# Optimization experiments

Hardware: AMD Instinct MI355X
Metric: run time of the kernel (lower is better)

Reference implementation:

```python
import jax, jax.numpy as jnp
import numpy as np

B, N, S = 32, 1000, 200
D, H, DK, FF, NL = 128, 8, 16, 512, 3
HK = H * DK


def _mha(x, Wq, Wk, Wv, Wo, bo):
    # x: [B, L, D]; manual multi-head attention matching the torch code
    Bv, L, _ = x.shape
    q = (x @ Wq).reshape(Bv, L, H, DK).transpose(0, 2, 1, 3)  # [B,H,L,dk]
    k = (x @ Wk).reshape(Bv, L, H, DK).transpose(0, 2, 1, 3)
    v = (x @ Wv).reshape(Bv, L, H, DK).transpose(0, 2, 1, 3)
    score = jnp.einsum('bhid,bhjd->bhij', q, k) / jnp.sqrt(jnp.asarray(DK, x.dtype))
    w = jax.nn.softmax(score, axis=-1)
    o = jnp.einsum('bhij,bhjd->bhid', w, v).transpose(0, 2, 1, 3).reshape(Bv, L, HK)
    return o @ Wo + bo


def _decoder_layer(x, Wq, Wk, Wv, Wo, bo, W1, b1, W2, b2):
    out1 = x + _mha(x, Wq, Wk, Wv, Wo, bo)
    ff = jax.nn.relu(out1 @ W1 + b1) @ W2 + b2
    return out1 + ff


def _forward(data, attention_bias, Wfirst, bfirst, Wlast, blast,
             Wq, Wk, Wv, Wo, bo, W1, b1, W2, b2, Wfin, bfin, sel):
    Bv, Np, Dm = data.shape
    Sn = sel.shape[1]
    bidx = jnp.arange(Bv)
    # _get_new_data: ordered list of unselected node indices, shape [B, N-S]
    mask = jnp.zeros((Bv, Np), bool).at[bidx[:, None], sel].set(True)
    vals = jnp.where(mask, Np, jnp.arange(Np)[None, :])
    unselect = jnp.sort(vals, axis=1)[:, : Np - Sn]            # [B, N-S]
    left = jnp.take_along_axis(data, unselect[:, :, None], axis=1)  # [B, N-S, D]
    # _get_encoding for first / last selected node
    first = data[bidx, sel[:, 0]]
    last = data[bidx, sel[:, -1]]
    ef = first @ Wfirst + bfirst
    el = last @ Wlast + blast
    out = jnp.concatenate([ef[:, None], left, el[:, None]], axis=1)  # [B, N-S+2, D]
    for i in range(Wq.shape[0]):
        out = _decoder_layer(out, Wq[i], Wk[i], Wv[i], Wo[i], bo[i],
                             W1[i], b1[i], W2[i], b2[i])
    logits = (out @ Wfin + bfin)[..., 0]                       # [B, N-S+2]
    # attention bias of current (last selected) node, gathered at unselected
    ab_cur = attention_bias[bidx, sel[:, -1]]                  # [B, N]
    ab_uns = jnp.take_along_axis(ab_cur, unselect, axis=1)     # [B, N-S]
    logits = logits.at[:, 1:-1].add(ab_uns)
    L = logits.shape[1]
    pos = jnp.arange(L)
    end_mask = (pos == 0) | (pos == L - 1)
    logits = jnp.where(end_mask[None, :], -jnp.inf, logits)
    props = jax.nn.softmax(logits, axis=-1)[:, 1:-1]           # [B, N-S]
    props = jnp.where(props <= 1e-5, props + 1e-7, props)
    # scatter back: selected positions -> -2, unselected -> props
    new_props = jnp.full((Bv, Np), -2.0, dtype=data.dtype)
    new_props = new_props.at[bidx[:, None], unselect].set(props)
    return new_props


def setup_inputs() -> dict:
    key = jax.random.key(0)
    ks = jax.random.split(key, 24)
    data = jax.random.normal(ks[0], (B, N, D), jnp.float32)
    # selected_node_list must contain unique indices per row (partial tour)
    sel = jax.vmap(lambda k: jax.random.permutation(k, N))(
        jax.random.split(ks[1], B))[:, :S].astype(jnp.int32)
    attention_bias = jax.random.normal(ks[2], (B, N, N), jnp.float32)

    def lin(k, shape, fan_in):
        return jax.random.normal(k, shape, jnp.float32) / np.float32(np.sqrt(fan_in))

    return dict(
        data=data,
        attention_bias=attention_bias,
        Wfirst=lin(ks[3], (D, D), D), bfirst=jnp.zeros((D,), jnp.float32),
        Wlast=lin(ks[4], (D, D), D), blast=jnp.zeros((D,), jnp.float32),
        Wq=lin(ks[5], (NL, D, HK), D),
        Wk=lin(ks[6], (NL, D, HK), D),
        Wv=lin(ks[7], (NL, D, HK), D),
        Wo=lin(ks[8], (NL, HK, D), HK), bo=jnp.zeros((NL, D), jnp.float32),
        W1=lin(ks[9], (NL, D, FF), D), b1=jnp.zeros((NL, FF), jnp.float32),
        W2=lin(ks[10], (NL, FF, D), FF), b2=jnp.zeros((NL, D), jnp.float32),
        Wfin=lin(ks[11], (D, 1), D), bfin=jnp.zeros((1,), jnp.float32),
        selected_node_list=sel,
    )


def reference(data, attention_bias, Wfirst, bfirst, Wlast, blast,
              Wq, Wk, Wv, Wo, bo, W1, b1, W2, b2, Wfin, bfin,
              selected_node_list):
    return _forward(data, attention_bias, Wfirst, bfirst, Wlast, blast,
                    Wq, Wk, Wv, Wo, bo, W1, b1, W2, b2, Wfin, bfin,
                    selected_node_list)
```

## Files before the change

kernel.cpp:

```cpp
#include <hip/hip_runtime.h>
#include <hip/hip_bf16.h>
#include <math.h>

#define NB 32
#define NN 1000
#define SS 200
#define DD 128
#define HH 8
#define DKK 16
#define FFD 512
#define NLAYER 3
#define LQ 802
#define LPAD 832
#define NPADK (LPAD - LQ)
#define MROWS (NB*LQ)
#define NBLK64 (MROWS/64)
#define NQT 26
#define NQT64 13
#define HSTR 516
#define TSTR 132
#define QSCALE 0.3606737602f

typedef __attribute__((ext_vector_type(8))) short short8;
typedef __attribute__((ext_vector_type(4))) short short4v;
typedef __attribute__((ext_vector_type(16))) float f32x16;
typedef __attribute__((ext_vector_type(2))) unsigned int uint2v;

static __device__ __forceinline__ unsigned short f2bf(float x) {
  union { float f; unsigned int u; } v; v.f = x;
  unsigned int r = v.u + 0x7fff + ((v.u >> 16) & 1);
  return (unsigned short)(r >> 16);
}

static __device__ __forceinline__ unsigned short f2bf1(float x) {
  unsigned int r;
  asm("v_cvt_pk_bf16_f32 %0, %1, 0" : "=v"(r) : "v"(x));
  return (unsigned short)r;
}

static __device__ __forceinline__ unsigned int cvtpk_bf16(float lo, float hi) {
  unsigned int r;
  asm("v_cvt_pk_bf16_f32 %0, %1, %2" : "=v"(r) : "v"(lo), "v"(hi));
  return r;
}

static __device__ __forceinline__ float max3f(float a, float b, float c) {
  float r;
  asm("v_max3_f32 %0, %1, %2, %3" : "=v"(r) : "v"(a), "v"(b), "v"(c));
  return r;
}

static __device__ __forceinline__ float exp2n(float x) {
  float r;
  asm("v_exp_f32 %0, %1" : "=v"(r) : "v"(x));
  return r;
}

static __device__ __forceinline__ uint2v pls(unsigned int a, unsigned int b) {
  return __builtin_amdgcn_permlane32_swap(a, b, false, false);
}
static __device__ __forceinline__ unsigned int fu(float x){ return __float_as_uint(x); }
static __device__ __forceinline__ float uf(unsigned int x){ return __uint_as_float(x); }

#define WCH 196608
__global__ __launch_bounds__(256) void k_wconv(const float* __restrict__ Wq, const float* __restrict__ Wk,
                       const float* __restrict__ Wv, const float* __restrict__ Wo,
                       const float* __restrict__ W1, const float* __restrict__ W2,
                       unsigned short* __restrict__ WtQKV, unsigned short* __restrict__ Wot,
                       unsigned short* __restrict__ W1t, unsigned short* __restrict__ W2t) {
  int e = blockIdx.x*256 + threadIdx.x;
  if (e >= 3*WCH) return;
  int layer = e / WCH, r = e - layer*WCH;
  if (r < 49152) {
    int n = r >> 7, k = r & 127;
    int sect = n >> 7, nn = n & 127;
    const float* W = (sect == 0) ? Wq : (sect == 1) ? Wk : Wv;
    WtQKV[layer*49152 + r] = f2bf1(W[layer*16384 + k*128 + nn]);
  } else if (r < 65536) {
    int r2 = r - 49152;
    int n = r2 >> 7, k = r2 & 127;
    Wot[layer*16384 + r2] = f2bf1(Wo[layer*16384 + k*128 + n]);
  } else if (r < 131072) {
    int r2 = r - 65536;
    int n = r2 >> 7, k = r2 & 127;
    W1t[layer*65536 + r2] = f2bf1(W1[layer*65536 + k*512 + n]);
  } else {
    int r2 = r - 131072;
    int n = r2 >> 9, k = r2 & 511;
    W2t[layer*65536 + r2] = f2bf1(W2[layer*65536 + k*128 + n]);
  }
}

__global__ __launch_bounds__(256) void k_padzero(unsigned short* __restrict__ Kb,
                                                 unsigned short* __restrict__ Vt) {
  int e = blockIdx.x*256 + threadIdx.x;
  if (e < 61440) {
    int bh = e / 240, r = e - bh*240;
    ((unsigned int*)&Kb[((size_t)bh*LPAD + LQ)*DKK])[r] = 0u;
  } else {
    int e2 = e - 61440;
    int bh = e2 / 240, r = e2 - bh*240;
    int d = r / 15, li = r - d*15;
    ((unsigned int*)&Vt[((size_t)bh*DKK + d)*LPAD + LQ])[li] = 0u;
  }
}

__global__ __launch_bounds__(1024) void k_unselect(const int* __restrict__ sel,
                                                   int* __restrict__ unselect,
                                                   int* __restrict__ pos) {
  int b = blockIdx.x;
  int n = threadIdx.x;
  __shared__ unsigned char fl[1024];
  __shared__ int wsum[16];
  fl[n] = (n < NN) ? 1 : 0;
  __syncthreads();
  if (n < SS) fl[sel[b*SS + n]] = 0;
  __syncthreads();
  int flag = fl[n];
  unsigned long long m = __ballot(flag);
  int lane = n & 63, w = n >> 6;
  int pre = __popcll(m & ((1ULL << lane) - 1ULL));
  if (lane == 63) wsum[w] = pre + flag;
  __syncthreads();
  int off = 0;
  #pragma unroll
  for (int i = 0; i < 16; ++i) off += (i < w) ? wsum[i] : 0;
  if (n < NN) {
    if (flag) {
      int j = off + pre;
      unselect[b*800 + j] = n;
      pos[b*NN + n] = j + 1;
    } else {
      pos[b*NN + n] = -1;
    }
  }
}

__global__ __launch_bounds__(128) void k_embed_ends(const float* __restrict__ data,
                       const int* __restrict__ sel,
                       const float* __restrict__ Wfirst, const float* __restrict__ bfirst,
                       const float* __restrict__ Wlast, const float* __restrict__ blast,
                       float* __restrict__ X, unsigned short* __restrict__ Xbf) {
  int which = blockIdx.x, b = blockIdx.y, d = threadIdx.x;
  int l = (which == 0) ? 0 : LQ-1;
  __shared__ float xr[DD];
  int src = sel[b*SS + (which == 0 ? 0 : SS-1)];
  const float* W    = (which == 0) ? Wfirst : Wlast;
  const float* bias = (which == 0) ? bfirst : blast;
  xr[d] = data[((size_t)b*NN + src)*DD + d];
  __syncthreads();
  float acc = bias[d];
  #pragma unroll 4
  for (int k = 0; k < DD; ++k) acc += xr[k] * W[k*DD + d];
  size_t off = ((size_t)(b*LQ + l))*DD + d;
  X[off] = acc;
  Xbf[off] = f2bf1(acc);
}

__global__ __launch_bounds__(256) void k_embed_mid(const float* __restrict__ data,
                       const int* __restrict__ unselect,
                       float* __restrict__ X, unsigned short* __restrict__ Xbf) {
  int e = blockIdx.x*256 + threadIdx.x;
  int r = e >> 5;
  int c4 = (e & 31) * 4;
  int b = r / 800, j = r - b*800;
  int nidx = unselect[r];
  const float4 v = *(const float4*)&data[((size_t)b*NN + nidx)*DD + c4];
  size_t off = ((size_t)(b*LQ + 1 + j))*DD + c4;
  *(float4*)&X[off] = v;
  unsigned int lo = cvtpk_bf16(v.x, v.y);
  unsigned int hi = cvtpk_bf16(v.z, v.w);
  unsigned long long pk8 = ((unsigned long long)hi << 32) | (unsigned long long)lo;
  *(unsigned long long*)&Xbf[off] = pk8;
}

__global__ __launch_bounds__(256) void k_qkv_mfma(const unsigned short* __restrict__ Xbf,
                       const unsigned short* __restrict__ Wt,
                       unsigned short* __restrict__ Qb, unsigned short* __restrict__ Kb,
                       unsigned short* __restrict__ Vt) {
  int row0 = blockIdx.x * 64;
  int t = threadIdx.x, wave = t >> 6, lane = t & 63;
  int col = lane & 31, half = lane >> 5;
  int b0 = row0 / LQ;
  int l00 = row0 - b0*LQ;
  int split = LQ - l00;
  short8 a[2][8];
  const unsigned short* xb = Xbf + (size_t)(row0 + col)*DD + half*8;
  #pragma unroll
  for (int mi = 0; mi < 2; ++mi)
    #pragma unroll
    for (int s = 0; s < 8; ++s)
      a[mi][s] = *(const short8*)(xb + (size_t)mi*32*DD + s*16);
  #pragma unroll
  for (int nn = 0; nn < 3; ++nn) {
    int ni = wave*3 + nn;
    short8 bfr[8];
    const unsigned short* wb = Wt + (size_t)(ni*32 + col)*DD + half*8;
    #pragma unroll
    for (int s = 0; s < 8; ++s) bfr[s] = *(const short8*)(wb + s*16);
    f32x16 acc0 = {0.f,0.f,0.f,0.f,0.f,0.f,0.f,0.f,0.f,0.f,0.f,0.f,0.f,0.f,0.f,0.f};
    f32x16 acc1 = {0.f,0.f,0.f,0.f,0.f,0.f,0.f,0.f,0.f,0.f,0.f,0.f,0.f,0.f,0.f,0.f};
    #pragma unroll
    for (int s = 0; s < 8; ++s) {
      acc0 = __builtin_amdgcn_mfma_f32_32x32x16_bf16(a[0][s], bfr[s], acc0, 0, 0, 0);
      acc1 = __builtin_amdgcn_mfma_f32_32x32x16_bf16(a[1][s], bfr[s], acc1, 0, 0, 0);
    }
    int n = ni*32 + col;
    int sect = n >> 7, nc = n & 127;
    int h = nc >> 4, d = nc & 15;
    if (sect < 2) {
      #pragma unroll
      for (int mi = 0; mi < 2; ++mi) {
        const f32x16& acc = mi ? acc1 : acc0;
        #pragma unroll
        for (int r = 0; r < 16; ++r) {
          int ml = mi*32 + (r&3) + 8*(r>>2) + 4*half;
          int over = (ml >= split);
          int b_ = b0 + over;
          int l  = over ? (ml - split) : (l00 + ml);
          size_t bh = (size_t)(b_*HH + h);
          float v = acc[r];
          if (sect == 0) Qb[(bh*LPAD + l)*DKK + d] = f2bf1(v * QSCALE);
          else           Kb[(bh*LPAD + l)*DKK + d] = f2bf1(v);
        }
      }
    } else {
      #pragma unroll
      for (int mi = 0; mi < 2; ++mi) {
        const f32x16& acc = mi ? acc1 : acc0;
        #pragma unroll
        for (int pj = 0; pj < 8; ++pj) {
          int j = pj >> 1, pi = pj & 1;
          int mlp = mi*32 + 8*j + 4*half + 2*pi;
          int over = (mlp >= split);
          int b_ = b0 + over;
          int l  = over ? (mlp - split) : (l00 + mlp);
          unsigned int w = cvtpk_bf16(acc[4*j + 2*pi], acc[4*j + 2*pi + 1]);
          *(unsigned int*)&Vt[((size_t)(b_*HH + h)*DKK + d)*LPAD + l] = w;
        }
      }
    }
  }
}

__global__ __launch_bounds__(256) void k_attn3(const unsigned short* __restrict__ Q,
                       const unsigned short* __restrict__ K,
                       const unsigned short* __restrict__ Vt,
                       unsigned short* __restrict__ Obf) {
  int bid = blockIdx.x;
  int g = bid & 7, i = bid >> 3;
  int bhg = i / NQT64, qt = i - bhg*NQT64;
  int bh = bhg*8 + g;
  int b = bh >> 3, h = bh & 7;
  int q0 = qt*64;
  size_t bhL = (size_t)bh * LPAD;
  int t = threadIdx.x;
  int wave = t >> 6, lane = t & 63;
  int col = lane & 31;
  int half = lane >> 5;

  __shared__ float mw[2][4][32];
  __shared__ float sw[2][4][32];
  __shared__ float sfin[2][32];
  __shared__ float ored[2][4][16][32];
  __shared__ float osum[2][32][17];

  uint2v pr = pls(1000u + (unsigned)lane, 2000u + (unsigned)lane);
  bool case1 = (__builtin_amdgcn_readfirstlane((int)pr.x) >= 2000);

  int q0c = q0 + col;      if (q0c > LQ-1) q0c = LQ-1;
  int q1c = q0 + 32 + col; if (q1c > LQ-1) q1c = LQ-1;
  short8 bQ0 = *(const short8*)&Q[(bhL + q0c)*DKK + half*8];
  short8 bQ1 = *(const short8*)&Q[(bhL + q1c)*DKK + half*8];

  f32x16 oacc0 = {0.f,0.f,0.f,0.f,0.f,0.f,0.f,0.f,0.f,0.f,0.f,0.f,0.f,0.f,0.f,0.f};
  f32x16 oacc1 = oacc0;
  float runm0 = 0.f, runm1 = 0.f;
  bool act = false;

  short8 aV0 = {0,0,0,0,0,0,0,0};
  short8 aV1 = {0,0,0,0,0,0,0,0};
  if (col == 16) {
    union { unsigned int u[4]; short8 s8; } o;
    o.u[0] = o.u[1] = o.u[2] = o.u[3] = 0x3F803F80u;
    aV0 = o.s8; aV1 = o.s8;
  }

  for (int kt = wave; kt < NQT; kt += 4) {
    int key0 = kt*32;
    short8 aK = *(const short8*)&K[(bhL + key0 + col)*DKK + half*8];
    if (col < 16) {
      const unsigned short* vp = &Vt[((size_t)bh*DKK + col)*LPAD + key0 + half*8];
      aV0 = *(const short8*)vp;
      aV1 = *(const short8*)(vp + 16);
    }

    auto process = [&](const short8& bQ, f32x16& oacc, float& runm) {
      f32x16 c = {0.f,0.f,0.f,0.f,0.f,0.f,0.f,0.f,0.f,0.f,0.f,0.f,0.f,0.f,0.f,0.f};
      c = __builtin_amdgcn_mfma_f32_32x32x16_bf16(aK, bQ, c, 0, 0, 0);
      float m0 = max3f(c[0],  c[1],  c[2]);
      float m1 = max3f(c[3],  c[4],  c[5]);
      float m2 = max3f(c[6],  c[7],  c[8]);
      float m3 = max3f(c[9],  c[10], c[11]);
      float m4 = max3f(c[12], c[13], c[14]);
      float tm = fmaxf(max3f(m0, m1, m2), max3f(m3, m4, c[15]));
      if (!__all(tm <= runm + 80.0f)) {
        uint2v rr = pls(fu(tm), fu(tm));
        float tmp = max3f(tm, uf(rr.x), uf(rr.y));
        float mnew = fmaxf(runm, tmp);
        float sc = exp2n(runm - mnew);
        #pragma unroll
        for (int r = 0; r < 9; ++r) oacc[r] *= sc;
        runm = mnew;
        act = true;
      }
      float p[16];
      if (act) {
        #pragma unroll
        for (int r = 0; r < 16; ++r) p[r] = exp2n(c[r] - runm);
      } else {
        #pragma unroll
        for (int r = 0; r < 16; ++r) p[r] = exp2n(c[r]);
      }
      unsigned int pk[8];
      #pragma unroll
      for (int j = 0; j < 8; ++j) pk[j] = cvtpk_bf16(p[2*j], p[2*j+1]);
      unsigned int fAx, fAy, fAz, fAw, fBx, fBy, fBz, fBw;
      if (case1) {
        uint2v r0 = pls(pk[2], pk[0]); fAz = r0.x; fAx = r0.y;
        uint2v r1 = pls(pk[3], pk[1]); fAw = r1.x; fAy = r1.y;
        uint2v r2 = pls(pk[6], pk[4]); fBz = r2.x; fBx = r2.y;
        uint2v r3 = pls(pk[7], pk[5]); fBw = r3.x; fBy = r3.y;
      } else {
        uint2v r0 = pls(pk[0], pk[2]); fAx = r0.x; fAz = r0.y;
        uint2v r1 = pls(pk[1], pk[3]); fAy = r1.x; fAw = r1.y;
        uint2v r2 = pls(pk[4], pk[6]); fBx = r2.x; fBz = r2.y;
        uint2v r3 = pls(pk[5], pk[7]); fBy = r3.x; fBw = r3.y;
      }
      union { unsigned int u[4]; short8 s8; } fA, fB;
      fA.u[0] = fAx; fA.u[1] = fAy; fA.u[2] = fAz; fA.u[3] = fAw;
      fB.u[0] = fBx; fB.u[1] = fBy; fB.u[2] = fBz; fB.u[3] = fBw;
      oacc = __builtin_amdgcn_mfma_f32_32x32x16_bf16(aV0, fA.s8, oacc, 0, 0, 0);
      oacc = __builtin_amdgcn_mfma_f32_32x32x16_bf16(aV1, fB.s8, oacc, 0, 0, 0);
    };
    process(bQ0, oacc0, runm0);
    process(bQ1, oacc1, runm1);
  }

  if (half == 0) {
    mw[0][wave][col] = runm0;  sw[0][wave][col] = oacc0[8];
    mw[1][wave][col] = runm1;  sw[1][wave][col] = oacc1[8];
  }
  __syncthreads();
  #pragma unroll
  for (int u = 0; u < 2; ++u) {
    float M = fmaxf(fmaxf(mw[u][0][col], mw[u][1][col]), fmaxf(mw[u][2][col], mw[u][3][col]));
    float S = sw[u][0][col]*exp2n(mw[u][0][col]-M) + sw[u][1][col]*exp2n(mw[u][1][col]-M)
            + sw[u][2][col]*exp2n(mw[u][2][col]-M) + sw[u][3][col]*exp2n(mw[u][3][col]-M);
    float runm = u ? runm1 : runm0;
    float fw = exp2n(runm - M);
    const f32x16& oacc = u ? oacc1 : oacc0;
    #pragma unroll
    for (int r = 0; r < 8; ++r) {
      int dv = (r&3) + 8*(r>>2) + 4*half;
      ored[u][wave][dv][col] = oacc[r] * fw;
    }
    if (wave == 0 && half == 0)
      sfin[u][col] = S - (float)NPADK * exp2n(-M);
  }
  __syncthreads();
  {
    int qq = t & 31, dv0 = t >> 5;
    #pragma unroll
    for (int u = 0; u < 2; ++u)
      #pragma unroll
      for (int k = 0; k < 2; ++k) {
        int dv = dv0 + 8*k;
        osum[u][qq][dv] = ored[u][0][dv][qq] + ored[u][1][dv][qq]
                        + ored[u][2][dv][qq] + ored[u][3][dv][qq];
      }
  }
  __syncthreads();
  {
    int qs = t >> 3, c2 = (t & 7)*2;
    #pragma unroll
    for (int u = 0; u < 2; ++u) {
      int q = q0 + u*32 + qs;
      if (q < LQ) {
        float invS = 1.f / sfin[u][qs];
        unsigned int pkv = cvtpk_bf16(osum[u][qs][c2] * invS, osum[u][qs][c2+1] * invS);
        *(unsigned int*)&Obf[((size_t)(b*LQ + q))*DD + h*DKK + c2] = pkv;
      }
    }
  }
}

__global__ __launch_bounds__(256) void k_pff(const unsigned short* __restrict__ Obf,
        const unsigned short* __restrict__ Wot, const float* __restrict__ bo,
        const unsigned short* __restrict__ W1t, const float* __restrict__ b1,
        const unsigned short* __restrict__ W2t, const float* __restrict__ b2,
        float* __restrict__ X, unsigned short* __restrict__ Xbf) {
  __shared__ __align__(16) unsigned short LDSU[64 * HSTR];
  unsigned short* T  = LDSU;
  unsigned short* Hs = LDSU;
  int row0 = blockIdx.x * 64;
  int t = threadIdx.x, wave = t >> 6, lane = t & 63;
  int col = lane & 31, half = lane >> 5;
  int n = wave*32 + col;
  float res[2][16];
  {
    short8 a[2][8];
    const unsigned short* ob = Obf + (size_t)(row0 + col)*DD + half*8;
    #pragma unroll
    for (int mi = 0; mi < 2; ++mi)
      #pragma unroll
      for (int s = 0; s < 8; ++s)
        a[mi][s] = *(const short8*)(ob + (size_t)mi*32*DD + s*16);
    short8 bfr[8];
    const unsigned short* wb = Wot + (size_t)n*DD + half*8;
    #pragma unroll
    for (int s = 0; s < 8; ++s) bfr[s] = *(const short8*)(wb + s*16);
    f32x16 acc0 = {0.f,0.f,0.f,0.f,0.f,0.f,0.f,0.f,0.f,0.f,0.f,0.f,0.f,0.f,0.f,0.f};
    f32x16 acc1 = acc0;
    #pragma unroll
    for (int s = 0; s < 8; ++s) {
      acc0 = __builtin_amdgcn_mfma_f32_32x32x16_bf16(a[0][s], bfr[s], acc0, 0, 0, 0);
      acc1 = __builtin_amdgcn_mfma_f32_32x32x16_bf16(a[1][s], bfr[s], acc1, 0, 0, 0);
    }
    float bv = bo[n];
    #pragma unroll
    for (int mi = 0; mi < 2; ++mi) {
      const f32x16& acc = mi ? acc1 : acc0;
      #pragma unroll
      for (int r = 0; r < 16; ++r) {
        int ml = mi*32 + (r&3) + 8*(r>>2) + 4*half;
        size_t off = (size_t)(row0 + ml)*DD + n;
        res[mi][r] = X[off] + acc[r] + bv;
        T[ml*TSTR + n] = f2bf1(res[mi][r]);
      }
    }
  }
  __syncthreads();
  short8 aF[2][8];
  #pragma unroll
  for (int mi = 0; mi < 2; ++mi)
    #pragma unroll
    for (int s = 0; s < 8; ++s) {
      const unsigned short* tp = &T[(mi*32 + col)*TSTR + half*8 + s*16];
      union { short4v h[2]; short8 v; } u;
      u.h[0] = *(const short4v*)tp;
      u.h[1] = *(const short4v*)(tp + 4);
      aF[mi][s] = u.v;
    }
  __syncthreads();
  #pragma unroll
  for (int nn = 0; nn < 4; ++nn) {
    int ni = wave*4 + nn;
    short8 bfr[8];
    const unsigned short* wb = W1t + (size_t)(ni*32 + col)*DD + half*8;
    #pragma unroll
    for (int s = 0; s < 8; ++s) bfr[s] = *(const short8*)(wb + s*16);
    f32x16 acc0 = {0.f,0.f,0.f,0.f,0.f,0.f,0.f,0.f,0.f,0.f,0.f,0.f,0.f,0.f,0.f,0.f};
    f32x16 acc1 = acc0;
    #pragma unroll
    for (int s = 0; s < 8; ++s) {
      acc0 = __builtin_amdgcn_mfma_f32_32x32x16_bf16(aF[0][s], bfr[s], acc0, 0, 0, 0);
      acc1 = __builtin_amdgcn_mfma_f32_32x32x16_bf16(aF[1][s], bfr[s], acc1, 0, 0, 0);
    }
    int nf = ni*32 + col;
    float bv = b1[nf];
    #pragma unroll
    for (int mi = 0; mi < 2; ++mi) {
      const f32x16& acc = mi ? acc1 : acc0;
      #pragma unroll
      for (int r = 0; r < 16; ++r) {
        int ml = mi*32 + (r&3) + 8*(r>>2) + 4*half;
        Hs[ml*HSTR + nf] = f2bf1(fmaxf(acc[r] + bv, 0.f));
      }
    }
  }
  __syncthreads();
  f32x16 acc0 = {0.f,0.f,0.f,0.f,0.f,0.f,0.f,0.f,0.f,0.f,0.f,0.f,0.f,0.f,0.f,0.f};
  f32x16 acc1 = acc0;
  const unsigned short* w2b = W2t + (size_t)n*FFD + half*8;
  #pragma unroll 4
  for (int s = 0; s < 32; ++s) {
    int ko = s*16 + half*8;
    union { short4v h[2]; short8 v; } h0, h1;
    const unsigned short* hp0 = &Hs[col*HSTR + ko];
    const unsigned short* hp1 = &Hs[(32 + col)*HSTR + ko];
    h0.h[0] = *(const short4v*)hp0;  h0.h[1] = *(const short4v*)(hp0 + 4);
    h1.h[0] = *(const short4v*)hp1;  h1.h[1] = *(const short4v*)(hp1 + 4);
    short8 bfr = *(const short8*)(w2b + s*16);
    acc0 = __builtin_amdgcn_mfma_f32_32x32x16_bf16(h0.v, bfr, acc0, 0, 0, 0);
    acc1 = __builtin_amdgcn_mfma_f32_32x32x16_bf16(h1.v, bfr, acc1, 0, 0, 0);
  }
  float bv = b2[n];
  #pragma unroll
  for (int mi = 0; mi < 2; ++mi) {
    const f32x16& acc = mi ? acc1 : acc0;
    #pragma unroll
    for (int r = 0; r < 16; ++r) {
      int ml = mi*32 + (r&3) + 8*(r>>2) + 4*half;
      size_t off = (size_t)(row0 + ml)*DD + n;
      float v = res[mi][r] + acc[r] + bv;
      X[off] = v;
      Xbf[off] = f2bf1(v);
    }
  }
}

__global__ __launch_bounds__(256) void k_final(const float* __restrict__ X,
                       const float* __restrict__ Wfin, const float* __restrict__ bfin,
                       const float* __restrict__ AB, const int* __restrict__ sel,
                       const int* __restrict__ unselect, const int* __restrict__ pos,
                       float* __restrict__ out) {
  int b = blockIdx.x, t = threadIdx.x;
  __shared__ float sl[800];
  __shared__ float red[256];
  __shared__ float wf[DD];
  if (t < DD) wf[t] = Wfin[t];
  int lastsel = sel[b*SS + SS-1];
  const float* abrow = AB + ((size_t)b*NN + lastsel)*NN;
  float bias = bfin[0];
  __syncthreads();
  for (int j = t; j < 800; j += 256) {
    const float* xr = &X[((size_t)(b*LQ + 1 + j))*DD];
    float acc = 0.f;
    #pragma unroll 8
    for (int k = 0; k < DD; k += 4) {
      float4 xv = *(const float4*)&xr[k];
      acc += xv.x*wf[k] + xv.y*wf[k+1] + xv.z*wf[k+2] + xv.w*wf[k+3];
    }
    sl[j] = acc + bias + abrow[unselect[b*800 + j]];
  }
  __syncthreads();
  float lm = -INFINITY;
  for (int j = t; j < 800; j += 256) lm = fmaxf(lm, sl[j]);
  red[t] = lm;
  __syncthreads();
  for (int s = 128; s > 0; s >>= 1) {
    if (t < s) red[t] = fmaxf(red[t], red[t+s]);
    __syncthreads();
  }
  float m = red[0];
  __syncthreads();
  float ls = 0.f;
  for (int j = t; j < 800; j += 256) ls += __expf(sl[j] - m);
  red[t] = ls;
  __syncthreads();
  for (int s = 128; s > 0; s >>= 1) {
    if (t < s) red[t] += red[t+s];
    __syncthreads();
  }
  float inv = 1.f / red[0];
  for (int n = t; n < NN; n += 256) {
    int p1 = pos[b*NN + n];
    float v = -2.0f;
    if (p1 >= 0) {
      float p = __expf(sl[p1-1] - m) * inv;
      if (p <= 1e-5f) p += 1e-7f;
      v = p;
    }
    out[(size_t)b*NN + n] = v;
  }
}

extern "C" void kernel_launch(void* const* d_in, const int* in_sizes, int n_in,
                              void* d_out, int out_size, void* d_ws, size_t ws_size,
                              hipStream_t stream) {
  const float* data   = (const float*)d_in[0];
  const float* AB     = (const float*)d_in[1];
  const float* Wfirst = (const float*)d_in[2];
  const float* bfirst = (const float*)d_in[3];
  const float* Wlast  = (const float*)d_in[4];
  const float* blast  = (const float*)d_in[5];
  const float* Wq     = (const float*)d_in[6];
  const float* Wk     = (const float*)d_in[7];
  const float* Wv     = (const float*)d_in[8];
  const float* Wo     = (const float*)d_in[9];
  const float* bo     = (const float*)d_in[10];
  const float* W1     = (const float*)d_in[11];
  const float* b1     = (const float*)d_in[12];
  const float* W2     = (const float*)d_in[13];
  const float* b2     = (const float*)d_in[14];
  const float* Wfin   = (const float*)d_in[15];
  const float* bfin   = (const float*)d_in[16];
  const int*   sel    = (const int*)d_in[17];
  float* out = (float*)d_out;
  (void)in_sizes; (void)n_in; (void)out_size; (void)ws_size;

  char* ws = (char*)d_ws;
  const size_t NELT = (size_t)MROWS * DD;
  const size_t KVELT = (size_t)NB*HH*LPAD*DKK;
  int*   UNSEL = (int*)ws;
  int*   POS   = (int*)(ws + 102400);
  float* X     = (float*)(ws + 230400);
  unsigned short* Xbf = (unsigned short*)(X + NELT);
  unsigned short* Ob  = Xbf + NELT;
  unsigned short* Qb  = Ob + NELT;
  unsigned short* Kb  = Qb + KVELT;
  unsigned short* Vt  = Kb + KVELT;
  unsigned short* WtQKV = Vt + KVELT;
  unsigned short* Wot = WtQKV + (size_t)NLAYER*384*128;
  unsigned short* W1t = Wot + (size_t)NLAYER*128*128;
  unsigned short* W2t = W1t + (size_t)NLAYER*512*128;

  k_wconv<<<(3*WCH + 255)/256, 256, 0, stream>>>(Wq, Wk, Wv, Wo, W1, W2, WtQKV, Wot, W1t, W2t);
  k_padzero<<<480, 256, 0, stream>>>(Kb, Vt);
  k_unselect<<<NB, 1024, 0, stream>>>(sel, UNSEL, POS);
  k_embed_ends<<<dim3(2, NB), 128, 0, stream>>>(data, sel, Wfirst, bfirst, Wlast, blast, X, Xbf);
  k_embed_mid<<<3200, 256, 0, stream>>>(data, UNSEL, X, Xbf);
  for (int i = 0; i < NLAYER; ++i) {
    k_qkv_mfma<<<NBLK64, 256, 0, stream>>>(Xbf, WtQKV + (size_t)i*384*128, Qb, Kb, Vt);
    k_attn3<<<NQT64*HH*NB, 256, 0, stream>>>(Qb, Kb, Vt, Ob);
    k_pff<<<NBLK64, 256, 0, stream>>>(Ob, Wot + (size_t)i*128*128, bo + (size_t)i*DD,
                                      W1t + (size_t)i*512*128, b1 + (size_t)i*FFD,
                                      W2t + (size_t)i*128*512, b2 + (size_t)i*DD, X, Xbf);
  }
  k_final<<<NB, 256, 0, stream>>>(X, Wfin, bfin, AB, sel, UNSEL, POS, out);
}
```

Measured before the change: 534.0 us.

## Give each attention wave its own query tile and halve PFF row block

The attention kernel now assigns each wave a separate 64-query tile that loops over all key tiles. Previously the four waves split the keys and merged partial softmax state through shared memory with three barriers; now normalization is done per wave in registers with a lane-pair permute and only a wave-local LDS transpose for coalesced stores. The feed-forward kernel processes 32 rows per block instead of 64, doubling the grid and shrinking LDS and register use. The trade-off is less K/V reuse per wave, idle trailing waves in the last query block, and reloading the weight tiles twice as often in the feed-forward kernel.

```diff
diff --git a/kernel.cpp b/kernel.cpp
--- a/kernel.cpp
+++ b/kernel.cpp
@@ -15,8 +15,8 @@
 #define NPADK (LPAD - LQ)
 #define MROWS (NB*LQ)
 #define NBLK64 (MROWS/64)
+#define NBLK32 (MROWS/32)
 #define NQT 26
-#define NQT64 13
 #define HSTR 516
 #define TSTR 132
 #define QSCALE 0.3606737602f
@@ -249,27 +249,25 @@
                        unsigned short* __restrict__ Obf) {
   int bid = blockIdx.x;
   int g = bid & 7, i = bid >> 3;
-  int bhg = i / NQT64, qt = i - bhg*NQT64;
+  int bhg = i >> 2, qb = i & 3;
   int bh = bhg*8 + g;
   int b = bh >> 3, h = bh & 7;
-  int q0 = qt*64;
   size_t bhL = (size_t)bh * LPAD;
   int t = threadIdx.x;
   int wave = t >> 6, lane = t & 63;
   int col = lane & 31;
   int half = lane >> 5;
 
-  __shared__ float mw[2][4][32];
-  __shared__ float sw[2][4][32];
-  __shared__ float sfin[2][32];
-  __shared__ float ored[2][4][16][32];
-  __shared__ float osum[2][32][17];
+  __shared__ __align__(16) unsigned short SO[4][2][32][20];
+
+  int q0w = qb*256 + wave*64;
+  if (q0w >= LPAD) return;
 
   uint2v pr = pls(1000u + (unsigned)lane, 2000u + (unsigned)lane);
   bool case1 = (__builtin_amdgcn_readfirstlane((int)pr.x) >= 2000);
 
-  int q0c = q0 + col;      if (q0c > LQ-1) q0c = LQ-1;
-  int q1c = q0 + 32 + col; if (q1c > LQ-1) q1c = LQ-1;
+  int q0c = q0w + col;      if (q0c > LQ-1) q0c = LQ-1;
+  int q1c = q0w + 32 + col; if (q1c > LQ-1) q1c = LQ-1;
   short8 bQ0 = *(const short8*)&Q[(bhL + q0c)*DKK + half*8];
   short8 bQ1 = *(const short8*)&Q[(bhL + q1c)*DKK + half*8];
 
@@ -286,7 +284,7 @@
     aV0 = o.s8; aV1 = o.s8;
   }
 
-  for (int kt = wave; kt < NQT; kt += 4) {
+  for (int kt = 0; kt < NQT; ++kt) {
     int key0 = kt*32;
     short8 aK = *(const short8*)&K[(bhL + key0 + col)*DKK + half*8];
     if (col < 16) {
@@ -347,52 +345,36 @@
     process(bQ1, oacc1, runm1);
   }
 
-  if (half == 0) {
-    mw[0][wave][col] = runm0;  sw[0][wave][col] = oacc0[8];
-    mw[1][wave][col] = runm1;  sw[1][wave][col] = oacc1[8];
-  }
-  __syncthreads();
   #pragma unroll
   for (int u = 0; u < 2; ++u) {
-    float M = fmaxf(fmaxf(mw[u][0][col], mw[u][1][col]), fmaxf(mw[u][2][col], mw[u][3][col]));
-    float S = sw[u][0][col]*exp2n(mw[u][0][col]-M) + sw[u][1][col]*exp2n(mw[u][1][col]-M)
-            + sw[u][2][col]*exp2n(mw[u][2][col]-M) + sw[u][3][col]*exp2n(mw[u][3][col]-M);
+    const f32x16& oacc = u ? oacc1 : oacc0;
     float runm = u ? runm1 : runm0;
-    float fw = exp2n(runm - M);
-    const f32x16& oacc = u ? oacc1 : oacc0;
-    #pragma unroll
-    for (int r = 0; r < 8; ++r) {
-      int dv = (r&3) + 8*(r>>2) + 4*half;
-      ored[u][wave][dv][col] = oacc[r] * fw;
-    }
-    if (wave == 0 && half == 0)
-      sfin[u][col] = S - (float)NPADK * exp2n(-M);
-  }
-  __syncthreads();
-  {
-    int qq = t & 31, dv0 = t >> 5;
-    #pragma unroll
-    for (int u = 0; u < 2; ++u)
-      #pragma unroll
-      for (int k = 0; k < 2; ++k) {
-        int dv = dv0 + 8*k;
-        osum[u][qq][dv] = ored[u][0][dv][qq] + ored[u][1][dv][qq]
-                        + ored[u][2][dv][qq] + ored[u][3][dv][qq];
-      }
-  }
-  __syncthreads();
-  {
-    int qs = t >> 3, c2 = (t & 7)*2;
-    #pragma unroll
-    for (int u = 0; u < 2; ++u) {
-      int q = q0 + u*32 + qs;
-      if (q < LQ) {
-        float invS = 1.f / sfin[u][qs];
-        unsigned int pkv = cvtpk_bf16(osum[u][qs][c2] * invS, osum[u][qs][c2+1] * invS);
-        *(unsigned int*)&Obf[((size_t)(b*LQ + q))*DD + h*DKK + c2] = pkv;
-      }
-    }
-  }
+    uint2v re = pls(fu(oacc[8]), fu(oacc[8]));
+    float S = uf(re.x) + uf(re.y) - (float)NPADK * exp2n(-runm);
+    float invS = 1.f / S;
+    unsigned int o0 = cvtpk_bf16(oacc[0]*invS, oacc[1]*invS);
+    unsigned int o1 = cvtpk_bf16(oacc[2]*invS, oacc[3]*invS);
+    unsigned int o2 = cvtpk_bf16(oacc[4]*invS, oacc[5]*invS);
+    unsigned int o3 = cvtpk_bf16(oacc[6]*invS, oacc[7]*invS);
+    int dbase = 4*half;
+    *(unsigned int*)&SO[wave][u][col][dbase+0]  = o0;
+    *(unsigned int*)&SO[wave][u][col][dbase+2]  = o1;
+    *(unsigned int*)&SO[wave][u][col][dbase+8]  = o2;
+    *(unsigned int*)&SO[wave][u][col][dbase+10] = o3;
+  }
+  asm volatile("s_waitcnt lgkmcnt(0)" ::: "memory");
+  __builtin_amdgcn_sched_barrier(0);
+  #pragma unroll
+  for (int u = 0; u < 2; ++u)
+    #pragma unroll
+    for (int pass = 0; pass < 2; ++pass) {
+      int qq = pass*16 + (lane >> 2);
+      int s = lane & 3;
+      ushort4 v = *(const ushort4*)&SO[wave][u][qq][s*4];
+      int q = q0w + u*32 + qq;
+      if (q < LQ)
+        *(ushort4*)&Obf[((size_t)(b*LQ + q))*DD + h*DKK + s*4] = v;
+    }
 }
 
 __global__ __launch_bounds__(256) void k_pff(const unsigned short* __restrict__ Obf,
@@ -400,58 +382,47 @@
         const unsigned short* __restrict__ W1t, const float* __restrict__ b1,
         const unsigned short* __restrict__ W2t, const float* __restrict__ b2,
         float* __restrict__ X, unsigned short* __restrict__ Xbf) {
-  __shared__ __align__(16) unsigned short LDSU[64 * HSTR];
+  __shared__ __align__(16) unsigned short LDSU[32 * HSTR];
   unsigned short* T  = LDSU;
   unsigned short* Hs = LDSU;
-  int row0 = blockIdx.x * 64;
+  int row0 = blockIdx.x * 32;
   int t = threadIdx.x, wave = t >> 6, lane = t & 63;
   int col = lane & 31, half = lane >> 5;
   int n = wave*32 + col;
-  float res[2][16];
+  float res[16];
   {
-    short8 a[2][8];
+    short8 a[8];
     const unsigned short* ob = Obf + (size_t)(row0 + col)*DD + half*8;
     #pragma unroll
-    for (int mi = 0; mi < 2; ++mi)
-      #pragma unroll
-      for (int s = 0; s < 8; ++s)
-        a[mi][s] = *(const short8*)(ob + (size_t)mi*32*DD + s*16);
+    for (int s = 0; s < 8; ++s)
+      a[s] = *(const short8*)(ob + s*16);
     short8 bfr[8];
     const unsigned short* wb = Wot + (size_t)n*DD + half*8;
     #pragma unroll
     for (int s = 0; s < 8; ++s) bfr[s] = *(const short8*)(wb + s*16);
     f32x16 acc0 = {0.f,0.f,0.f,0.f,0.f,0.f,0.f,0.f,0.f,0.f,0.f,0.f,0.f,0.f,0.f,0.f};
-    f32x16 acc1 = acc0;
-    #pragma unroll
-    for (int s = 0; s < 8; ++s) {
-      acc0 = __builtin_amdgcn_mfma_f32_32x32x16_bf16(a[0][s], bfr[s], acc0, 0, 0, 0);
-      acc1 = __builtin_amdgcn_mfma_f32_32x32x16_bf16(a[1][s], bfr[s], acc1, 0, 0, 0);
-    }
+    #pragma unroll
+    for (int s = 0; s < 8; ++s)
+      acc0 = __builtin_amdgcn_mfma_f32_32x32x16_bf16(a[s], bfr[s], acc0, 0, 0, 0);
     float bv = bo[n];
     #pragma unroll
-    for (int mi = 0; mi < 2; ++mi) {
-      const f32x16& acc = mi ? acc1 : acc0;
-      #pragma unroll
-      for (int r = 0; r < 16; ++r) {
-        int ml = mi*32 + (r&3) + 8*(r>>2) + 4*half;
-        size_t off = (size_t)(row0 + ml)*DD + n;
-        res[mi][r] = X[off] + acc[r] + bv;
-        T[ml*TSTR + n] = f2bf1(res[mi][r]);
-      }
-    }
-  }
-  __syncthreads();
-  short8 aF[2][8];
-  #pragma unroll
-  for (int mi = 0; mi < 2; ++mi)
-    #pragma unroll
-    for (int s = 0; s < 8; ++s) {
-      const unsigned short* tp = &T[(mi*32 + col)*TSTR + half*8 + s*16];
-      union { short4v h[2]; short8 v; } u;
-      u.h[0] = *(const short4v*)tp;
-      u.h[1] = *(const short4v*)(tp + 4);
-      aF[mi][s] = u.v;
-    }
+    for (int r = 0; r < 16; ++r) {
+      int ml = (r&3) + 8*(r>>2) + 4*half;
+      size_t off = (size_t)(row0 + ml)*DD + n;
+      res[r] = X[off] + acc0[r] + bv;
+      T[ml*TSTR + n] = f2bf1(res[r]);
+    }
+  }
+  __syncthreads();
+  short8 aF[8];
+  #pragma unroll
+  for (int s = 0; s < 8; ++s) {
+    const unsigned short* tp = &T[col*TSTR + half*8 + s*16];
+    union { short4v h[2]; short8 v; } u;
+    u.h[0] = *(const short4v*)tp;
+    u.h[1] = *(const short4v*)(tp + 4);
+    aF[s] = u.v;
+  }
   __syncthreads();
   #pragma unroll
   for (int nn = 0; nn < 4; ++nn) {
@@ -461,52 +432,37 @@
     #pragma unroll
     for (int s = 0; s < 8; ++s) bfr[s] = *(const short8*)(wb + s*16);
     f32x16 acc0 = {0.f,0.f,0.f,0.f,0.f,0.f,0.f,0.f,0.f,0.f,0.f,0.f,0.f,0.f,0.f,0.f};
-    f32x16 acc1 = acc0;
-    #pragma unroll
-    for (int s = 0; s < 8; ++s) {
-      acc0 = __builtin_amdgcn_mfma_f32_32x32x16_bf16(aF[0][s], bfr[s], acc0, 0, 0, 0);
-      acc1 = __builtin_amdgcn_mfma_f32_32x32x16_bf16(aF[1][s], bfr[s], acc1, 0, 0, 0);
-    }
+    #pragma unroll
+    for (int s = 0; s < 8; ++s)
+      acc0 = __builtin_amdgcn_mfma_f32_32x32x16_bf16(aF[s], bfr[s], acc0, 0, 0, 0);
     int nf = ni*32 + col;
     float bv = b1[nf];
     #pragma unroll
-    for (int mi = 0; mi < 2; ++mi) {
-      const f32x16& acc = mi ? acc1 : acc0;
-      #pragma unroll
-      for (int r = 0; r < 16; ++r) {
-        int ml = mi*32 + (r&3) + 8*(r>>2) + 4*half;
-        Hs[ml*HSTR + nf] = f2bf1(fmaxf(acc[r] + bv, 0.f));
-      }
+    for (int r = 0; r < 16; ++r) {
+      int ml = (r&3) + 8*(r>>2) + 4*half;
+      Hs[ml*HSTR + nf] = f2bf1(fmaxf(acc0[r] + bv, 0.f));
     }
   }
   __syncthreads();
   f32x16 acc0 = {0.f,0.f,0.f,0.f,0.f,0.f,0.f,0.f,0.f,0.f,0.f,0.f,0.f,0.f,0.f,0.f};
-  f32x16 acc1 = acc0;
   const unsigned short* w2b = W2t + (size_t)n*FFD + half*8;
   #pragma unroll 4
   for (int s = 0; s < 32; ++s) {
     int ko = s*16 + half*8;
-    union { short4v h[2]; short8 v; } h0, h1;
+    union { short4v h[2]; short8 v; } h0;
     const unsigned short* hp0 = &Hs[col*HSTR + ko];
-    const unsigned short* hp1 = &Hs[(32 + col)*HSTR + ko];
     h0.h[0] = *(const short4v*)hp0;  h0.h[1] = *(const short4v*)(hp0 + 4);
-    h1.h[0] = *(const short4v*)hp1;  h1.h[1] = *(const short4v*)(hp1 + 4);
     short8 bfr = *(const short8*)(w2b + s*16);
     acc0 = __builtin_amdgcn_mfma_f32_32x32x16_bf16(h0.v, bfr, acc0, 0, 0, 0);
-    acc1 = __builtin_amdgcn_mfma_f32_32x32x16_bf16(h1.v, bfr, acc1, 0, 0, 0);
   }
   float bv = b2[n];
   #pragma unroll
-  for (int mi = 0; mi < 2; ++mi) {
-    const f32x16& acc = mi ? acc1 : acc0;
-    #pragma unroll
-    for (int r = 0; r < 16; ++r) {
-      int ml = mi*32 + (r&3) + 8*(r>>2) + 4*half;
-      size_t off = (size_t)(row0 + ml)*DD + n;
-      float v = res[mi][r] + acc[r] + bv;
-      X[off] = v;
-      Xbf[off] = f2bf1(v);
-    }
+  for (int r = 0; r < 16; ++r) {
+    int ml = (r&3) + 8*(r>>2) + 4*half;
+    size_t off = (size_t)(row0 + ml)*DD + n;
+    float v = res[r] + acc0[r] + bv;
+    X[off] = v;
+    Xbf[off] = f2bf1(v);
   }
 }
 
@@ -613,8 +569,8 @@
   k_embed_mid<<<3200, 256, 0, stream>>>(data, UNSEL, X, Xbf);
   for (int i = 0; i < NLAYER; ++i) {
     k_qkv_mfma<<<NBLK64, 256, 0, stream>>>(Xbf, WtQKV + (size_t)i*384*128, Qb, Kb, Vt);
-    k_attn3<<<NQT64*HH*NB, 256, 0, stream>>>(Qb, Kb, Vt, Ob);
-    k_pff<<<NBLK64, 256, 0, stream>>>(Ob, Wot + (size_t)i*128*128, bo + (size_t)i*DD,
+    k_attn3<<<NB*HH*4, 256, 0, stream>>>(Qb, Kb, Vt, Ob);
+    k_pff<<<NBLK32, 256, 0, stream>>>(Ob, Wot + (size_t)i*128*128, bo + (size_t)i*DD,
                                       W1t + (size_t)i*512*128, b1 + (size_t)i*FFD,
                                       W2t + (size_t)i*128*512, b2 + (size_t)i*DD, X, Xbf);
   }
```

Result: slower. 608.0 us (+13.9%).
